# Kernel optimization log

Hardware: AMD Instinct MI355X
Metric: run time of the kernel (lower is better)

The kernel has to match this reference:

```python
import jax, jax.numpy as jnp
import numpy as np

D, H, L, FF, IN, OUT, S, B = 512, 8, 6, 2048, 32, 3, 512, 32


def setup_inputs() -> dict:
    key = jax.random.key(0)
    ks = iter(jax.random.split(key, 32))
    w = lambda shape: jax.random.normal(next(ks), shape, jnp.float32) * 0.02
    z = lambda shape: jnp.zeros(shape, jnp.float32)
    o = lambda shape: jnp.ones(shape, jnp.float32)
    return {
        'x': jax.random.normal(next(ks), (B, S, IN), jnp.float32),
        'w_in': w((IN, D)), 'b_in': z((D,)), 'g_in': o((D,)), 'be_in': z((D,)),
        'w_qkv': w((L, D, 3 * D)), 'b_qkv': z((L, 3 * D)),
        'w_out': w((L, D, D)), 'b_out': z((L, D)),
        'g1': o((L, D)), 'be1': z((L, D)),
        'w_ff1': w((L, D, FF)), 'b_ff1': z((L, FF)),
        'w_ff2': w((L, FF, D)), 'b_ff2': z((L, D)),
        'g2': o((L, D)), 'be2': z((L, D)),
        'w_h1': w((D, D // 2)), 'b_h1': z((D // 2,)),
        'w_h2': w((D // 2, OUT)), 'b_h2': z((OUT,)),
    }


def _layer_norm(x, g, b, eps=1e-5):
    mu = jnp.mean(x, axis=-1, keepdims=True)
    var = jnp.mean(jnp.square(x - mu), axis=-1, keepdims=True)
    return (x - mu) / jnp.sqrt(var + eps) * g + b


def _gelu(x):
    return jax.nn.gelu(x, approximate=False)  # torch nn.GELU default (erf)


def _pos_encoding(seq_len, d_model):
    pos = jnp.arange(seq_len, dtype=jnp.float32)[:, None]
    div = jnp.exp(jnp.arange(0, d_model, 2, dtype=jnp.float32) * (-np.log(10000.0) / d_model))
    pe = jnp.zeros((seq_len, d_model), jnp.float32)
    pe = pe.at[:, 0::2].set(jnp.sin(pos * div))
    pe = pe.at[:, 1::2].set(jnp.cos(pos * div))
    return pe


def reference(x, w_in, b_in, g_in, be_in, w_qkv, b_qkv, w_out, b_out,
              g1, be1, w_ff1, b_ff1, w_ff2, b_ff2, g2, be2,
              w_h1, b_h1, w_h2, b_h2):
    b, s, _ = x.shape
    d = w_in.shape[1]
    hd = d // H
    scale = hd ** -0.5

    # input projection: Linear -> LayerNorm -> GELU (dropout = identity at eval)
    h = _gelu(_layer_norm(x @ w_in + b_in, g_in, be_in))
    h = h + _pos_encoding(s, d)

    causal_mask = jnp.triu(jnp.ones((s, s), bool), 1)  # True above diagonal = future

    for l in range(w_qkv.shape[0]):
        qkv = (h @ w_qkv[l] + b_qkv[l]).reshape(b, s, 3, H, hd)
        q, k, v = qkv[:, :, 0], qkv[:, :, 1], qkv[:, :, 2]  # [b, s, H, hd]
        scores = jnp.einsum('bihd,bjhd->bhij', q, k) * scale
        scores = jnp.where(causal_mask, -jnp.inf, scores)
        attn = jax.nn.softmax(scores, axis=-1)
        o = jnp.einsum('bhij,bjhd->bihd', attn, v).reshape(b, s, d)
        o = o @ w_out[l] + b_out[l]
        h = _layer_norm(h + o, g1[l], be1[l])
        f = _gelu(h @ w_ff1[l] + b_ff1[l]) @ w_ff2[l] + b_ff2[l]
        h = _layer_norm(h + f, g2[l], be2[l])

    logits = _gelu(h @ w_h1 + b_h1) @ w_h2 + b_h2  # [b, s, OUT]
    return logits[:, -1, :]  # last position only
```

## Files before the change

### kernel.cpp

```cpp
#include <hip/hip_runtime.h>
#include <hip/hip_bf16.h>
#include <math.h>

#define D_   512
#define H_   8
#define HD_  64
#define L_   6
#define FF_  2048
#define IN_  32
#define OUT_ 3
#define S_   512
#define B_   32
#define M_   (B_ * S_)

typedef __attribute__((ext_vector_type(8))) short short8;
typedef __attribute__((ext_vector_type(4))) float floatx4;

__device__ __forceinline__ float gelu_f(float x) {
    const float ax = fabsf(x) * 0.70710678118654752f;
    const float t = __builtin_amdgcn_rcpf(fmaf(0.3275911f, ax, 1.0f));
    float p = fmaf(1.061405429f, t, -1.453152027f);
    p = fmaf(p, t, 1.421413741f);
    p = fmaf(p, t, -0.284496736f);
    p = fmaf(p, t, 0.254829592f);
    p = p * t;
    const float e = __expf(-ax * ax);
    const float er = copysignf(fmaf(-p, e, 1.0f), x);
    return 0.5f * x * (1.0f + er);
}
__device__ __forceinline__ float bf2f(unsigned short u) {
    union { unsigned int i; float f; } c; c.i = ((unsigned)u) << 16; return c.f;
}
__device__ __forceinline__ unsigned short f2bf(float v) {
    __hip_bfloat16 t = __float2bfloat16(v);
    return *(unsigned short*)&t;
}
__device__ __forceinline__ void async16(const void* g, void* l) {
    __builtin_amdgcn_global_load_lds(
        (const __attribute__((address_space(1))) unsigned int*)g,
        (__attribute__((address_space(3))) unsigned int*)l, 16, 0, 0);
}
__device__ __forceinline__ void stage2(const short* g, char* d, long rs, int off2) {
    async16(g, d);
    async16(g + rs, d + off2);
}


#define MFMA_ROW(ai, accr)                                                    \
    accr[0] = __builtin_amdgcn_mfma_f32_16x16x32_bf16(ai, b[0], accr[0], 0, 0, 0); \
    accr[1] = __builtin_amdgcn_mfma_f32_16x16x32_bf16(ai, b[1], accr[1], 0, 0, 0); \
    accr[2] = __builtin_amdgcn_mfma_f32_16x16x32_bf16(ai, b[2], accr[2], 0, 0, 0); \
    accr[3] = __builtin_amdgcn_mfma_f32_16x16x32_bf16(ai, b[3], accr[3], 0, 0, 0);

#define MFMA_PHASE(B0)                                                        \
    __builtin_amdgcn_s_barrier();                                             \
    asm volatile("s_waitcnt lgkmcnt(0)" ::: "memory");                        \
    __builtin_amdgcn_sched_barrier(0);                                        \
    __builtin_amdgcn_s_setprio(1);                                            \
    MFMA_ROW(a[0], acc[B0 + 0])                                               \
    MFMA_ROW(a[1], acc[B0 + 1])                                               \
    MFMA_ROW(a[2], acc[B0 + 2])                                               \
    MFMA_ROW(a[3], acc[B0 + 3])                                               \
    __builtin_amdgcn_s_setprio(0);

template<int DO_GELU, int OUT_BF16, int ADD_RES>
__global__ __launch_bounds__(512, 2)
void gemm_mfma256_k(const __hip_bfloat16* __restrict__ A,
                    const __hip_bfloat16* __restrict__ WT,
                    const float* __restrict__ bias,
                    const float* __restrict__ R,
                    void* __restrict__ C,
                    int N, int K) {
    __shared__ __align__(16) char smem[131072];

    const int tid  = threadIdx.x;
    const int lane = tid & 63;
    const int wave = tid >> 6;

    const int Lid = blockIdx.y * gridDim.x + blockIdx.x;
    const int xcd = Lid & 7;
    const int idx = Lid >> 3;
    const int gx  = gridDim.x, gy8 = gridDim.y >> 3;
    const int m0 = (xcd * gy8 + idx / gx) * 256;
    const int n0 = (idx % gx) * 256;

    const int wm = (wave >> 2) * 128;
    const int wn = (wave & 3) * 64;
    const int r = lane & 15, q = lane >> 4;
    const int qa = (q ^ ((r >> 1) & 3)) * 8;

    const int srow = tid >> 2;
    const int sc = ((tid & 3) ^ ((tid >> 3) & 3)) * 8;
    const short* Ag = (const short*)A + (long)(m0 + srow) * K + sc;
    const short* Bg = (const short*)WT + (long)(n0 + srow) * K + sc;
    const long rs = (long)128 * K;

    floatx4 acc[8][4];
    #pragma unroll
    for (int i = 0; i < 8; i++)
        #pragma unroll
        for (int j = 0; j < 4; j++) acc[i][j] = (floatx4)0.f;

    const int NT = K >> 6;

    stage2(Ag,      smem         + tid * 16, rs, 8192);
    stage2(Bg,      smem + 32768 + tid * 16, rs, 8192);
    stage2(Ag + 32, smem + 16384 + tid * 16, rs, 8192);
    stage2(Bg + 32, smem + 49152 + tid * 16, rs, 8192);
    asm volatile("s_waitcnt vmcnt(4)" ::: "memory");
    __builtin_amdgcn_s_barrier();

    short8 a[4], b[4];
    for (int t = 0; t < NT; ++t) {
        const int cur = t & 1, nxt = cur ^ 1;
        const bool hn = (t + 1 < NT);
        const short* As = (const short*)(smem + cur * 65536);
        const short* Bs = (const short*)(smem + cur * 65536 + 32768);
        const short* Agt = Ag + (t + 1) * 64;
        const short* Bgt = Bg + (t + 1) * 64;
        char* Ad = smem + nxt * 65536;
        char* Bd = smem + nxt * 65536 + 32768;

        #pragma unroll
        for (int i = 0; i < 4; i++)
            a[i] = *(const short8*)&As[(wm + i * 16 + r) * 32 + qa];
        #pragma unroll
        for (int j = 0; j < 4; j++)
            b[j] = *(const short8*)&Bs[(wn + j * 16 + r) * 32 + qa];
        if (hn) stage2(Agt, Ad + tid * 16, rs, 8192);
        MFMA_PHASE(0)
        __builtin_amdgcn_s_barrier();

        #pragma unroll
        for (int i = 0; i < 4; i++)
            a[i] = *(const short8*)&As[(wm + 64 + i * 16 + r) * 32 + qa];
        if (hn) stage2(Bgt, Bd + tid * 16, rs, 8192);
        MFMA_PHASE(4)
        if (hn) asm volatile("s_waitcnt vmcnt(4)" ::: "memory");
        else    asm volatile("s_waitcnt vmcnt(0)" ::: "memory");
        __builtin_amdgcn_s_barrier();

        #pragma unroll
        for (int i = 0; i < 4; i++)
            a[i] = *(const short8*)&As[8192 + (wm + i * 16 + r) * 32 + qa];
        #pragma unroll
        for (int j = 0; j < 4; j++)
            b[j] = *(const short8*)&Bs[8192 + (wn + j * 16 + r) * 32 + qa];
        if (hn) stage2(Agt + 32, Ad + 16384 + tid * 16, rs, 8192);
        MFMA_PHASE(0)
        __builtin_amdgcn_s_barrier();

        #pragma unroll
        for (int i = 0; i < 4; i++)
            a[i] = *(const short8*)&As[8192 + (wm + 64 + i * 16 + r) * 32 + qa];
        if (hn) stage2(Bgt + 32, Bd + 16384 + tid * 16, rs, 8192);
        MFMA_PHASE(4)
        if (hn) asm volatile("s_waitcnt vmcnt(4)" ::: "memory");
        __builtin_amdgcn_s_barrier();
    }

    float* Ef = (float*)smem;
    const int erow = tid >> 3;
    const int ej = tid & 7;
    #pragma unroll
    for (int ch = 0; ch < 4; ch++) {
        __builtin_amdgcn_s_barrier();
        if ((wave >> 2) == (ch >> 1)) {
            #pragma unroll
            for (int mf2 = 0; mf2 < 4; mf2++) {
                const int mf = (ch & 1) * 4 + mf2;
                #pragma unroll
                for (int nf = 0; nf < 4; nf++)
                    #pragma unroll
                    for (int rg = 0; rg < 4; rg++)
                        Ef[(mf2 * 16 + q * 4 + rg) * 260 + wn + nf * 16 + r] =
                            acc[mf][nf][rg];
            }
        }
        __builtin_amdgcn_s_barrier();
        #pragma unroll
        for (int e = 0; e < 8; e++) {
            const int c4 = ej + e * 8;
            const long grow = (long)(m0 + ch * 64 + erow) * N + n0 + c4 * 4;
            const float4 v = *(const float4*)&Ef[erow * 260 + c4 * 4];
            const float4 bv = *(const float4*)&bias[n0 + c4 * 4];
            float o0 = v.x + bv.x, o1 = v.y + bv.y;
            float o2 = v.z + bv.z, o3 = v.w + bv.w;
            if (DO_GELU) {
                o0 = gelu_f(o0); o1 = gelu_f(o1);
                o2 = gelu_f(o2); o3 = gelu_f(o3);
            }
            if (ADD_RES) {
                const float4 rv = *(const float4*)&R[grow];
                o0 += rv.x; o1 += rv.y; o2 += rv.z; o3 += rv.w;
            }
            if (OUT_BF16) {
                ushort4 pk;
                pk.x = f2bf(o0); pk.y = f2bf(o1);
                pk.z = f2bf(o2); pk.w = f2bf(o3);
                *(ushort4*)((unsigned short*)C + grow) = pk;
            } else {
                *(float4*)((float*)C + grow) = make_float4(o0, o1, o2, o3);
            }
        }
    }
}

template<int DO_GELU, int OUT_BF16, int ADD_RES>
__global__ __launch_bounds__(256, 2)
void gemm_mfma_k(const __hip_bfloat16* __restrict__ A,
                 const __hip_bfloat16* __restrict__ WT,
                 const float* __restrict__ bias,
                 const float* __restrict__ R,
                 void* __restrict__ C,
                 int N, int K) {
    __shared__ __align__(16) char smem[65536];
    float* Ep = (float*)smem;

    const int tid  = threadIdx.x;
    const int lane = tid & 63;
    const int wave = tid >> 6;

    const int Lid = blockIdx.y * gridDim.x + blockIdx.x;
    const int xcd = Lid & 7;
    const int idx = Lid >> 3;
    const int gx  = gridDim.x, gy8 = gridDim.y >> 3;
    const int m0 = (xcd * gy8 + idx / gx) * 128;
    const int n0 = (idx % gx) * 128;

    const int wm = (wave >> 1) * 64, wn = (wave & 1) * 64;
    const int r = lane & 15, q = lane >> 4;
    const int qa = (q ^ ((r >> 1) & 3)) * 8;

    const int srow = tid >> 2;
    const int sc = ((tid & 3) ^ ((tid >> 3) & 3)) * 8;
    const short* Ag = (const short*)A + (long)(m0 + srow) * K + sc;
    const short* Bg = (const short*)WT + (long)(n0 + srow) * K + sc;
    const long rs = (long)64 * K;

    floatx4 acc[4][4];
    #pragma unroll
    for (int i = 0; i < 4; i++)
        #pragma unroll
        for (int j = 0; j < 4; j++) acc[i][j] = (floatx4)0.f;

    const int NT = K >> 6;

    stage2(Ag,      smem + 0     + tid * 16, rs, 4096);
    stage2(Bg,      smem + 16384 + tid * 16, rs, 4096);
    stage2(Ag + 32, smem + 8192  + tid * 16, rs, 4096);
    stage2(Bg + 32, smem + 24576 + tid * 16, rs, 4096);
    asm volatile("s_waitcnt vmcnt(4)" ::: "memory");
    __builtin_amdgcn_s_barrier();
    __builtin_amdgcn_sched_barrier(0);

    short8 a[4], b[4];
    for (int t = 0; t < NT; ++t) {
        const int cur = t & 1, nxt = cur ^ 1;
        const bool hn = (t + 1 < NT);
        const short* As = (const short*)(smem + cur * 32768);
        const short* Bs = (const short*)(smem + cur * 32768 + 16384);
        const short* Agt = Ag + (t + 1) * 64;
        const short* Bgt = Bg + (t + 1) * 64;
        char* Ad = smem + nxt * 32768;
        char* Bd = smem + nxt * 32768 + 16384;

        if (hn) {
            stage2(Agt, Ad + tid * 16, rs, 4096);
            stage2(Bgt, Bd + tid * 16, rs, 4096);
        }
        #pragma unroll
        for (int i = 0; i < 4; i++)
            a[i] = *(const short8*)&As[(wm + i * 16 + r) * 32 + qa];
        #pragma unroll
        for (int j = 0; j < 4; j++)
            b[j] = *(const short8*)&Bs[(wn + j * 16 + r) * 32 + qa];
        #pragma unroll
        for (int i = 0; i < 4; i++)
            #pragma unroll
            for (int j = 0; j < 4; j++)
                acc[i][j] = __builtin_amdgcn_mfma_f32_16x16x32_bf16(
                    a[i], b[j], acc[i][j], 0, 0, 0);
        __builtin_amdgcn_sched_barrier(0);
        if (hn) asm volatile("s_waitcnt vmcnt(4)" ::: "memory");
        else    asm volatile("s_waitcnt vmcnt(0)" ::: "memory");
        __builtin_amdgcn_s_barrier();
        __builtin_amdgcn_sched_barrier(0);

        if (hn) {
            stage2(Agt + 32, Ad + 8192 + tid * 16, rs, 4096);
            stage2(Bgt + 32, Bd + 8192 + tid * 16, rs, 4096);
        }
        #pragma unroll
        for (int i = 0; i < 4; i++)
            a[i] = *(const short8*)&As[4096 + (wm + i * 16 + r) * 32 + qa];
        #pragma unroll
        for (int j = 0; j < 4; j++)
            b[j] = *(const short8*)&Bs[4096 + (wn + j * 16 + r) * 32 + qa];
        #pragma unroll
        for (int i = 0; i < 4; i++)
            #pragma unroll
            for (int j = 0; j < 4; j++)
                acc[i][j] = __builtin_amdgcn_mfma_f32_16x16x32_bf16(
                    a[i], b[j], acc[i][j], 0, 0, 0);
        __builtin_amdgcn_sched_barrier(0);
        if (hn) asm volatile("s_waitcnt vmcnt(4)" ::: "memory");
        __builtin_amdgcn_s_barrier();
        __builtin_amdgcn_sched_barrier(0);
    }

    const int erow = tid >> 5;
    const int ecol = (tid & 31) * 4;
    const float4 bvec = *(const float4*)&bias[n0 + ecol];

    #pragma unroll
    for (int pass = 0; pass < 2; pass++) {
        if (pass) __syncthreads();
        if ((wave >> 1) == pass) {
            #pragma unroll
            for (int i = 0; i < 4; i++)
                #pragma unroll
                for (int j = 0; j < 4; j++)
                    #pragma unroll
                    for (int rg = 0; rg < 4; rg++)
                        Ep[(i * 16 + q * 4 + rg) * 132 + wn + j * 16 + r] =
                            acc[i][j][rg];
        }
        __syncthreads();
        #pragma unroll
        for (int it = 0; it < 8; it++) {
            const int row = it * 8 + erow;
            const long grow = (long)(m0 + pass * 64 + row) * N + n0 + ecol;
            const float4 v = *(const float4*)&Ep[row * 132 + ecol];
            float o0 = v.x + bvec.x, o1 = v.y + bvec.y;
            float o2 = v.z + bvec.z, o3 = v.w + bvec.w;
            if (DO_GELU) {
                o0 = gelu_f(o0); o1 = gelu_f(o1);
                o2 = gelu_f(o2); o3 = gelu_f(o3);
            }
            if (ADD_RES) {
                const float4 rv = *(const float4*)&R[grow];
                o0 += rv.x; o1 += rv.y; o2 += rv.z; o3 += rv.w;
            }
            if (OUT_BF16) {
                ushort4 pk;
                pk.x = f2bf(o0); pk.y = f2bf(o1);
                pk.z = f2bf(o2); pk.w = f2bf(o3);
                *(ushort4*)((unsigned short*)C + grow) = pk;
            } else {
                *(float4*)((float*)C + grow) = make_float4(o0, o1, o2, o3);
            }
        }
    }
}

__global__ __launch_bounds__(256)
void transpose_cast_k(const float* __restrict__ W, __hip_bfloat16* __restrict__ WT,
                      int K, int N) {
    __shared__ float tile[32][33];
    const float* Wl = W + (long)blockIdx.z * K * N;
    __hip_bfloat16* WTl = WT + (long)blockIdx.z * K * N;
    const int n0 = blockIdx.x * 32, k0 = blockIdx.y * 32;
    const int tx = threadIdx.x & 31, ty = threadIdx.x >> 5;
    for (int rr = ty; rr < 32; rr += 8)
        tile[rr][tx] = Wl[(long)(k0 + rr) * N + n0 + tx];
    __syncthreads();
    for (int rr = ty; rr < 32; rr += 8)
        WTl[(long)(n0 + rr) * K + k0 + tx] = __float2bfloat16(tile[tx][rr]);
}

template<int DO_GELU>
__global__ __launch_bounds__(256)
void gemm_bias_k(const float* __restrict__ A, long lda,
                 const float* __restrict__ W,
                 const float* __restrict__ bias,
                 float* __restrict__ C,
                 int M, int N, int K) {
    __shared__ float As[16][64];
    __shared__ float Ws[16][64];
    const int tx = threadIdx.x;
    const int ty = threadIdx.y;
    const int tid = ty * 16 + tx;
    const int m0 = blockIdx.y * 64;
    const int n0 = blockIdx.x * 64;
    float acc[4][4] = {};
    for (int k0 = 0; k0 < K; k0 += 16) {
        #pragma unroll
        for (int e = tid; e < 64 * 16; e += 256) {
            int m = e >> 4, k = e & 15;
            float v = 0.f;
            if (m0 + m < M) v = A[(long)(m0 + m) * lda + k0 + k];
            As[k][m] = v;
        }
        #pragma unroll
        for (int e = tid; e < 16 * 64; e += 256) {
            int k = e >> 6, n = e & 63;
            float v = 0.f;
            if (n0 + n < N) v = W[(long)(k0 + k) * N + n0 + n];
            Ws[k][n] = v;
        }
        __syncthreads();
        #pragma unroll
        for (int kk = 0; kk < 16; kk++) {
            float a[4], w[4];
            #pragma unroll
            for (int i = 0; i < 4; i++) a[i] = As[kk][ty * 4 + i];
            #pragma unroll
            for (int j = 0; j < 4; j++) w[j] = Ws[kk][tx * 4 + j];
            #pragma unroll
            for (int i = 0; i < 4; i++)
                #pragma unroll
                for (int j = 0; j < 4; j++)
                    acc[i][j] += a[i] * w[j];
        }
        __syncthreads();
    }
    #pragma unroll
    for (int i = 0; i < 4; i++) {
        int m = m0 + ty * 4 + i;
        if (m >= M) continue;
        #pragma unroll
        for (int j = 0; j < 4; j++) {
            int n = n0 + tx * 4 + j;
            if (n >= N) continue;
            float v = acc[i][j] + bias[n];
            if (DO_GELU) v = gelu_f(v);
            C[(long)m * N + n] = v;
        }
    }
}

__global__ __launch_bounds__(256)
void ln_k(const float* __restrict__ X,
          const float* __restrict__ g,
          const float* __restrict__ be,
          float* __restrict__ H,
          __hip_bfloat16* __restrict__ Hb) {
    const int row = blockIdx.x * 4 + (threadIdx.x >> 6);
    const int lane = threadIdx.x & 63;
    const float* xp = X + (long)row * D_ + lane * 8;
    const float4 a = *(const float4*)xp;
    const float4 c = *(const float4*)(xp + 4);
    float s = a.x + a.y + a.z + a.w + c.x + c.y + c.z + c.w;
    #pragma unroll
    for (int off = 1; off < 64; off <<= 1) s += __shfl_xor(s, off);
    const float mu = s * (1.0f / D_);
    float d[8] = { a.x - mu, a.y - mu, a.z - mu, a.w - mu,
                   c.x - mu, c.y - mu, c.z - mu, c.w - mu };
    float ss = 0.f;
    #pragma unroll
    for (int e = 0; e < 8; e++) ss += d[e] * d[e];
    #pragma unroll
    for (int off = 1; off < 64; off <<= 1) ss += __shfl_xor(ss, off);
    const float inv = 1.0f / sqrtf(ss * (1.0f / D_) + 1e-5f);
    const float4 g0 = *(const float4*)(g + lane * 8);
    const float4 g1 = *(const float4*)(g + lane * 8 + 4);
    const float4 e0 = *(const float4*)(be + lane * 8);
    const float4 e1 = *(const float4*)(be + lane * 8 + 4);
    const float gv[8] = { g0.x, g0.y, g0.z, g0.w, g1.x, g1.y, g1.z, g1.w };
    const float ev[8] = { e0.x, e0.y, e0.z, e0.w, e1.x, e1.y, e1.z, e1.w };
    float o[8];
    short8 pk;
    #pragma unroll
    for (int e = 0; e < 8; e++) {
        o[e] = d[e] * inv * gv[e] + ev[e];
        pk[e] = (short)f2bf(o[e]);
    }
    float* hp = H + (long)row * D_ + lane * 8;
    *(float4*)hp = make_float4(o[0], o[1], o[2], o[3]);
    *(float4*)(hp + 4) = make_float4(o[4], o[5], o[6], o[7]);
    *(short8*)((unsigned short*)Hb + (long)row * D_ + lane * 8) = pk;
}

__global__ __launch_bounds__(256)
void ln_gelu_pos_k(const float* __restrict__ X,
                   const float* __restrict__ g,
                   const float* __restrict__ be,
                   float* __restrict__ Hout,
                   __hip_bfloat16* __restrict__ Hb) {
    const int row = blockIdx.x;
    const int s = row & (S_ - 1);
    const int t = threadIdx.x;
    const float* x = X + (long)row * D_;
    float v0 = x[t], v1 = x[t + 256];
    __shared__ float red[256];
    red[t] = v0 + v1;
    __syncthreads();
    for (int off = 128; off; off >>= 1) {
        if (t < off) red[t] += red[t + off];
        __syncthreads();
    }
    float mu = red[0] * (1.0f / D_);
    __syncthreads();
    float d0 = v0 - mu, d1 = v1 - mu;
    red[t] = d0 * d0 + d1 * d1;
    __syncthreads();
    for (int off = 128; off; off >>= 1) {
        if (t < off) red[t] += red[t + off];
        __syncthreads();
    }
    float var = red[0] * (1.0f / D_);
    float inv = 1.0f / sqrtf(var + 1e-5f);
    float o0 = gelu_f(d0 * inv * g[t] + be[t]);
    float o1 = gelu_f(d1 * inv * g[t + 256] + be[t + 256]);
    {
        int d = t, i = d >> 1;
        float dv = expf((float)(2 * i) * (-9.210340371976184f / 512.0f));
        float ang = (float)s * dv;
        o0 += (d & 1) ? cosf(ang) : sinf(ang);
    }
    {
        int d = t + 256, i = d >> 1;
        float dv = expf((float)(2 * i) * (-9.210340371976184f / 512.0f));
        float ang = (float)s * dv;
        o1 += (d & 1) ? cosf(ang) : sinf(ang);
    }
    Hout[(long)row * D_ + t] = o0;
    Hout[(long)row * D_ + t + 256] = o1;
    Hb[(long)row * D_ + t] = __float2bfloat16(o0);
    Hb[(long)row * D_ + t + 256] = __float2bfloat16(o1);
}

#define LDT 72
__global__ __launch_bounds__(256)
void attn_mfma_k(const __hip_bfloat16* __restrict__ qkv,
                 __hip_bfloat16* __restrict__ O) {
    const int qt = blockIdx.x;
    const int bh = blockIdx.y;
    const int b = bh >> 3, h = bh & (H_ - 1);
    const int tid = threadIdx.x;
    const int wave = tid >> 6, lane = tid & 63;
    const int ln = lane & 15, quad = lane >> 4;
    const int wm = wave * 32;
    const int i0 = qt * 128;

    __shared__ unsigned short Qs[128 * LDT];
    __shared__ unsigned short Ks[64 * LDT];
    __shared__ unsigned short Vt[64 * LDT];
    __shared__ unsigned short Ps[128 * LDT];
    __shared__ float stat[128];

    const unsigned short* base = (const unsigned short*)qkv + (long)b * S_ * (3 * D_);

    {
        const int r0 = tid >> 3, c0 = (tid & 7) * 8;
        #pragma unroll
        for (int i = 0; i < 4; i++) {
            const int rw = i * 32 + r0;
            *(short8*)&Qs[rw * LDT + c0] =
                *(const short8*)(base + (long)(i0 + rw) * (3 * D_) + h * HD_ + c0);
        }
    }

    float m_i[2] = { -INFINITY, -INFINITY };
    float l_i[2] = { 0.f, 0.f };
    floatx4 o_acc[2][4];
    #pragma unroll
    for (int i = 0; i < 2; i++)
        #pragma unroll
        for (int j = 0; j < 4; j++) o_acc[i][j] = (floatx4)0.f;

    const int kr = tid >> 2, kc = (tid & 3) * 16;
    const int vj = tid & 63, vc = (tid >> 6) * 16;

    const int ktmax = 2 * qt + 1;
    for (int kt = 0; kt <= ktmax; kt++) {
        const int j0 = kt * 64;
        {
            const unsigned short* kp = base + (long)(j0 + kr) * (3 * D_) + D_ + h * HD_ + kc;
            *(short8*)&Ks[kr * LDT + kc]     = *(const short8*)(kp);
            *(short8*)&Ks[kr * LDT + kc + 8] = *(const short8*)(kp + 8);
            const unsigned short* vp = base + (long)(j0 + vj) * (3 * D_) + 2 * D_ + h * HD_ + vc;
            short8 v0 = *(const short8*)(vp);
            short8 v1 = *(const short8*)(vp + 8);
            #pragma unroll
            for (int e = 0; e < 8; e++) {
                Vt[(vc + e) * LDT + vj]     = (unsigned short)v0[e];
                Vt[(vc + 8 + e) * LDT + vj] = (unsigned short)v1[e];
            }
        }
        __syncthreads();

        floatx4 sa[4][2];
        #pragma unroll
        for (int mt = 0; mt < 4; mt++)
            #pragma unroll
            for (int nt = 0; nt < 2; nt++) sa[mt][nt] = (floatx4)0.f;
        #pragma unroll
        for (int c = 0; c < 2; c++) {
            short8 kf[4], qf[2];
            #pragma unroll
            for (int mt = 0; mt < 4; mt++)
                kf[mt] = *(const short8*)&Ks[(mt * 16 + ln) * LDT + c * 32 + quad * 8];
            #pragma unroll
            for (int nt = 0; nt < 2; nt++)
                qf[nt] = *(const short8*)&Qs[(wm + nt * 16 + ln) * LDT + c * 32 + quad * 8];
            #pragma unroll
            for (int mt = 0; mt < 4; mt++)
                #pragma unroll
                for (int nt = 0; nt < 2; nt++)
                    sa[mt][nt] = __builtin_amdgcn_mfma_f32_16x16x32_bf16(
                        kf[mt], qf[nt], sa[mt][nt], 0, 0, 0);
        }

        const bool domask = (kt >= 2 * qt);
        #pragma unroll
        for (int nt = 0; nt < 2; nt++) {
            const int qg = i0 + wm + nt * 16 + ln;
            float mx = -INFINITY;
            #pragma unroll
            for (int mt = 0; mt < 4; mt++)
                #pragma unroll
                for (int rg = 0; rg < 4; rg++) {
                    float v = sa[mt][nt][rg] * 0.125f;
                    if (domask && (j0 + mt * 16 + quad * 4 + rg > qg)) v = -INFINITY;
                    sa[mt][nt][rg] = v;
                    mx = fmaxf(mx, v);
                }
            mx = fmaxf(mx, __shfl_xor(mx, 16));
            mx = fmaxf(mx, __shfl_xor(mx, 32));
            const float mn = fmaxf(m_i[nt], mx);
            const float alpha = __expf(m_i[nt] - mn);
            m_i[nt] = mn;
            float ls = 0.f;
            #pragma unroll
            for (int mt = 0; mt < 4; mt++) {
                ushort4 pk;
                float p0 = __expf(sa[mt][nt][0] - mn);
                float p1 = __expf(sa[mt][nt][1] - mn);
                float p2 = __expf(sa[mt][nt][2] - mn);
                float p3 = __expf(sa[mt][nt][3] - mn);
                ls += p0 + p1 + p2 + p3;
                pk.x = f2bf(p0); pk.y = f2bf(p1); pk.z = f2bf(p2); pk.w = f2bf(p3);
                *(ushort4*)&Ps[(wm + nt * 16 + ln) * LDT + mt * 16 + quad * 4] = pk;
            }
            ls += __shfl_xor(ls, 16);
            ls += __shfl_xor(ls, 32);
            l_i[nt] = l_i[nt] * alpha + ls;
            if (quad == 0) stat[wm + nt * 16 + ln] = alpha;
        }

        #pragma unroll
        for (int mt2 = 0; mt2 < 2; mt2++) {
            #pragma unroll
            for (int rg = 0; rg < 4; rg++) {
                const float a = stat[wm + mt2 * 16 + quad * 4 + rg];
                #pragma unroll
                for (int nt = 0; nt < 4; nt++) o_acc[mt2][nt][rg] *= a;
            }
        }

        #pragma unroll
        for (int c = 0; c < 2; c++) {
            short8 pf[2], vf[4];
            #pragma unroll
            for (int mt2 = 0; mt2 < 2; mt2++)
                pf[mt2] = *(const short8*)&Ps[(wm + mt2 * 16 + ln) * LDT + c * 32 + quad * 8];
            #pragma unroll
            for (int nt = 0; nt < 4; nt++)
                vf[nt] = *(const short8*)&Vt[(nt * 16 + ln) * LDT + c * 32 + quad * 8];
            #pragma unroll
            for (int mt2 = 0; mt2 < 2; mt2++)
                #pragma unroll
                for (int nt = 0; nt < 4; nt++)
                    o_acc[mt2][nt] = __builtin_amdgcn_mfma_f32_16x16x32_bf16(
                        pf[mt2], vf[nt], o_acc[mt2][nt], 0, 0, 0);
        }
        __syncthreads();
    }

    if (quad == 0) {
        stat[wm + ln]      = l_i[0];
        stat[wm + 16 + ln] = l_i[1];
    }
    unsigned short* Og = (unsigned short*)O;
    #pragma unroll
    for (int mt2 = 0; mt2 < 2; mt2++) {
        #pragma unroll
        for (int rg = 0; rg < 4; rg++) {
            const float linv = 1.0f / stat[wm + mt2 * 16 + quad * 4 + rg];
            const long row = (long)(b * S_ + i0 + wm + mt2 * 16 + quad * 4 + rg);
            #pragma unroll
            for (int nt = 0; nt < 4; nt++)
                Og[row * D_ + h * HD_ + nt * 16 + ln] =
                    f2bf(o_acc[mt2][nt][rg] * linv);
        }
    }
}

__global__ __launch_bounds__(256)
void head1_k(const float* __restrict__ h, const float* __restrict__ w1,
             const float* __restrict__ b1, float* __restrict__ th) {
    __shared__ float hs[D_];
    const int b = blockIdx.x, n = threadIdx.x;
    const float* hr = h + (long)(b * S_ + S_ - 1) * D_;
    hs[n] = hr[n];
    hs[n + 256] = hr[n + 256];
    __syncthreads();
    float s = 0.f;
    #pragma unroll 8
    for (int k = 0; k < D_; k++) s += hs[k] * w1[(long)k * 256 + n];
    th[b * 256 + n] = gelu_f(s + b1[n]);
}

__global__ __launch_bounds__(64)
void head2_k(const float* __restrict__ th, const float* __restrict__ w2,
             const float* __restrict__ b2, float* __restrict__ out) {
    const int b = blockIdx.x, lane = threadIdx.x;
    const float* t = th + b * 256;
    float s0 = 0.f, s1 = 0.f, s2 = 0.f;
    #pragma unroll
    for (int e = 0; e < 4; e++) {
        const int k = lane * 4 + e;
        const float tv = t[k];
        s0 += tv * w2[k * 3 + 0];
        s1 += tv * w2[k * 3 + 1];
        s2 += tv * w2[k * 3 + 2];
    }
    #pragma unroll
    for (int off = 1; off < 64; off <<= 1) {
        s0 += __shfl_xor(s0, off);
        s1 += __shfl_xor(s1, off);
        s2 += __shfl_xor(s2, off);
    }
    if (lane == 0) {
        out[b * 3 + 0] = s0 + b2[0];
        out[b * 3 + 1] = s1 + b2[1];
        out[b * 3 + 2] = s2 + b2[2];
    }
}

extern "C" void kernel_launch(void* const* d_in, const int* in_sizes, int n_in,
                              void* d_out, int out_size, void* d_ws, size_t ws_size,
                              hipStream_t stream) {
    const float* x     = (const float*)d_in[0];
    const float* w_in  = (const float*)d_in[1];
    const float* b_in  = (const float*)d_in[2];
    const float* g_in  = (const float*)d_in[3];
    const float* be_in = (const float*)d_in[4];
    const float* w_qkv = (const float*)d_in[5];
    const float* b_qkv = (const float*)d_in[6];
    const float* w_out = (const float*)d_in[7];
    const float* b_out = (const float*)d_in[8];
    const float* g1    = (const float*)d_in[9];
    const float* be1   = (const float*)d_in[10];
    const float* w_ff1 = (const float*)d_in[11];
    const float* b_ff1 = (const float*)d_in[12];
    const float* w_ff2 = (const float*)d_in[13];
    const float* b_ff2 = (const float*)d_in[14];
    const float* g2    = (const float*)d_in[15];
    const float* be2   = (const float*)d_in[16];
    const float* w_h1  = (const float*)d_in[17];
    const float* b_h1  = (const float*)d_in[18];
    const float* w_h2  = (const float*)d_in[19];
    const float* b_h2  = (const float*)d_in[20];
    float* out = (float*)d_out;

    float* h    = (float*)d_ws;
    float* bufB = h + (long)M_ * D_;
    float* th   = bufB + (long)M_ * D_;
    __hip_bfloat16* hb    = (__hip_bfloat16*)(th + 32 * 256);
    __hip_bfloat16* attb  = hb + (long)M_ * D_;
    __hip_bfloat16* bufAb = attb + (long)M_ * D_;
    __hip_bfloat16* qkvT  = bufAb + (long)M_ * FF_;
    __hip_bfloat16* outT  = qkvT + (long)L_ * (3 * D_) * D_;
    __hip_bfloat16* ff1T  = outT + (long)L_ * D_ * D_;
    __hip_bfloat16* ff2T  = ff1T + (long)L_ * FF_ * D_;

    dim3 blk(16, 16);

    transpose_cast_k<<<dim3((3 * D_) / 32, D_ / 32, L_), 256, 0, stream>>>(w_qkv, qkvT, D_, 3 * D_);
    transpose_cast_k<<<dim3(D_ / 32, D_ / 32, L_), 256, 0, stream>>>(w_out, outT, D_, D_);
    transpose_cast_k<<<dim3(FF_ / 32, D_ / 32, L_), 256, 0, stream>>>(w_ff1, ff1T, D_, FF_);
    transpose_cast_k<<<dim3(D_ / 32, FF_ / 32, L_), 256, 0, stream>>>(w_ff2, ff2T, FF_, D_);

    gemm_bias_k<0><<<dim3(D_ / 64, M_ / 64), blk, 0, stream>>>(
        x, IN_, w_in, b_in, bufB, M_, D_, IN_);
    ln_gelu_pos_k<<<M_, 256, 0, stream>>>(bufB, g_in, be_in, h, hb);

    for (int l = 0; l < L_; l++) {
        gemm_mfma_k<0, 1, 0><<<dim3((3 * D_) / 128, M_ / 128), 256, 0, stream>>>(
            hb, qkvT + (long)l * (3 * D_) * D_, b_qkv + l * 3 * D_, nullptr,
            bufAb, 3 * D_, D_);
        attn_mfma_k<<<dim3(S_ / 128, B_ * H_), 256, 0, stream>>>(bufAb, attb);
        gemm_mfma_k<0, 0, 1><<<dim3(D_ / 128, M_ / 128), 256, 0, stream>>>(
            attb, outT + (long)l * D_ * D_, b_out + l * D_, h,
            bufB, D_, D_);
        ln_k<<<M_ / 4, 256, 0, stream>>>(bufB, g1 + l * D_, be1 + l * D_, h, hb);
        gemm_mfma256_k<1, 1, 0><<<dim3(FF_ / 256, M_ / 256), 512, 0, stream>>>(
            hb, ff1T + (long)l * FF_ * D_, b_ff1 + l * FF_, nullptr,
            bufAb, FF_, D_);
        gemm_mfma_k<0, 0, 1><<<dim3(D_ / 128, M_ / 128), 256, 0, stream>>>(
            bufAb, ff2T + (long)l * D_ * FF_, b_ff2 + l * D_, h,
            bufB, D_, FF_);
        ln_k<<<M_ / 4, 256, 0, stream>>>(bufB, g2 + l * D_, be2 + l * D_, h, hb);
    }

    head1_k<<<B_, 256, 0, stream>>>(h, w_h1, b_h1, th);
    head2_k<<<B_, 64, 0, stream>>>(th, w_h2, b_h2, out);
}
```

Measured before the change: 1.688 ms.

## Fuse output/FF2 projection GEMMs with residual add and LayerNorm

Adds a GEMM kernel that computes full 64x512 output rows per block, so bias, residual add and LayerNorm run in the epilogue and write both fp32 and bf16 hidden states. It replaces the separate GEMM plus ln_k launches after attention and after FF2, removing the fp32 intermediate round trip and two launches per layer. In exchange it uses 256 blocks with about 144KB of LDS and one block per CU, so occupancy drops, and the layout is hardcoded to D=512. The residual R and the output Hout alias the same buffer h; this is safe only because each block reads its own rows before writing them.

```diff
diff --git a/kernel.cpp b/kernel.cpp
--- a/kernel.cpp
+++ b/kernel.cpp
@@ -350,6 +350,176 @@
             } else {
                 *(float4*)((float*)C + grow) = make_float4(o0, o1, o2, o3);
             }
+        }
+    }
+}
+
+__global__ __launch_bounds__(512, 1)
+void gemm_ln_k(const __hip_bfloat16* __restrict__ A,
+               const __hip_bfloat16* __restrict__ WT,
+               const float* __restrict__ bias,
+               const float* R,
+               const float* __restrict__ g,
+               const float* __restrict__ be,
+               float* Hout,
+               __hip_bfloat16* __restrict__ Hb,
+               int K) {
+    __shared__ __align__(16) char smem[147456];
+    const int tid  = threadIdx.x;
+    const int lane = tid & 63;
+    const int wave = tid >> 6;
+
+    const int Lid = blockIdx.x;
+    const int m0 = ((Lid & 7) * 32 + (Lid >> 3)) * 64;
+
+    const int wm2 = wave >> 2;
+    const int wn4 = wave & 3;
+    const int r = lane & 15, q = lane >> 4;
+    const int qaB  = (q ^ ((r >> 1) & 3)) * 8;
+    const int qaA0 = ((q)     ^ (r & 7)) * 8;
+    const int qaA1 = ((4 + q) ^ (r & 7)) * 8;
+
+    const int arow = tid >> 3;
+    const int asb  = ((tid & 7) ^ ((tid >> 3) & 7)) * 8;
+    const short* Ag = (const short*)A + (long)(m0 + arow) * K + asb;
+    const int brow = tid >> 2;
+    const int bsb  = ((tid & 3) ^ ((tid >> 3) & 3)) * 8;
+    const short* Bg = (const short*)WT + (long)brow * K + bsb;
+    const long brs = (long)128 * K;
+
+    floatx4 acc[2][8];
+    #pragma unroll
+    for (int i = 0; i < 2; i++)
+        #pragma unroll
+        for (int j = 0; j < 8; j++) acc[i][j] = (floatx4)0.f;
+
+    const int NTT = K >> 6;
+
+    {
+        char* base = smem;
+        async16(Ag, base + tid * 16);
+        const short* p0 = Bg;
+        char* d0 = base + 8192 + tid * 16;
+        async16(p0, d0); async16(p0 + brs, d0 + 8192);
+        async16(p0 + 2 * brs, d0 + 16384); async16(p0 + 3 * brs, d0 + 24576);
+        const short* p1 = Bg + 32;
+        char* d1 = base + 40960 + tid * 16;
+        async16(p1, d1); async16(p1 + brs, d1 + 8192);
+        async16(p1 + 2 * brs, d1 + 16384); async16(p1 + 3 * brs, d1 + 24576);
+    }
+    asm volatile("s_waitcnt vmcnt(4)" ::: "memory");
+    __builtin_amdgcn_s_barrier();
+    __builtin_amdgcn_sched_barrier(0);
+
+    for (int t = 0; t < NTT; ++t) {
+        const int cur = t & 1, nxt = cur ^ 1;
+        const bool hn = (t + 1 < NTT);
+        const short* As  = (const short*)(smem + cur * 73728);
+        const short* B0s = (const short*)(smem + cur * 73728 + 8192);
+        const short* B1s = (const short*)(smem + cur * 73728 + 40960);
+        char* nb = smem + nxt * 73728;
+        const long k1 = (long)(t + 1) * 64;
+
+        if (hn) {
+            async16(Ag + k1, nb + tid * 16);
+            const short* p0 = Bg + k1;
+            char* d0 = nb + 8192 + tid * 16;
+            async16(p0, d0); async16(p0 + brs, d0 + 8192);
+            async16(p0 + 2 * brs, d0 + 16384); async16(p0 + 3 * brs, d0 + 24576);
+        }
+        {
+            short8 a0 = *(const short8*)&As[(wm2 * 32 +      r) * 64 + qaA0];
+            short8 a1 = *(const short8*)&As[(wm2 * 32 + 16 + r) * 64 + qaA0];
+            short8 b[8];
+            #pragma unroll
+            for (int nf = 0; nf < 8; nf++)
+                b[nf] = *(const short8*)&B0s[(wn4 * 128 + nf * 16 + r) * 32 + qaB];
+            #pragma unroll
+            for (int nf = 0; nf < 8; nf++) {
+                acc[0][nf] = __builtin_amdgcn_mfma_f32_16x16x32_bf16(a0, b[nf], acc[0][nf], 0, 0, 0);
+                acc[1][nf] = __builtin_amdgcn_mfma_f32_16x16x32_bf16(a1, b[nf], acc[1][nf], 0, 0, 0);
+            }
+        }
+        __builtin_amdgcn_sched_barrier(0);
+        if (hn) asm volatile("s_waitcnt vmcnt(4)" ::: "memory");
+        else    asm volatile("s_waitcnt vmcnt(0)" ::: "memory");
+        __builtin_amdgcn_s_barrier();
+        __builtin_amdgcn_sched_barrier(0);
+
+        if (hn) {
+            const short* p1 = Bg + k1 + 32;
+            char* d1 = nb + 40960 + tid * 16;
+            async16(p1, d1); async16(p1 + brs, d1 + 8192);
+            async16(p1 + 2 * brs, d1 + 16384); async16(p1 + 3 * brs, d1 + 24576);
+        }
+        {
+            short8 a0 = *(const short8*)&As[(wm2 * 32 +      r) * 64 + qaA1];
+            short8 a1 = *(const short8*)&As[(wm2 * 32 + 16 + r) * 64 + qaA1];
+            short8 b[8];
+            #pragma unroll
+            for (int nf = 0; nf < 8; nf++)
+                b[nf] = *(const short8*)&B1s[(wn4 * 128 + nf * 16 + r) * 32 + qaB];
+            #pragma unroll
+            for (int nf = 0; nf < 8; nf++) {
+                acc[0][nf] = __builtin_amdgcn_mfma_f32_16x16x32_bf16(a0, b[nf], acc[0][nf], 0, 0, 0);
+                acc[1][nf] = __builtin_amdgcn_mfma_f32_16x16x32_bf16(a1, b[nf], acc[1][nf], 0, 0, 0);
+            }
+        }
+        __builtin_amdgcn_sched_barrier(0);
+        if (hn) asm volatile("s_waitcnt vmcnt(4)" ::: "memory");
+        __builtin_amdgcn_s_barrier();
+        __builtin_amdgcn_sched_barrier(0);
+    }
+
+    float* Ef = (float*)smem;
+    float* stat = (float*)(smem + 66816);
+    const float gl = g[tid], bl = be[tid], bv = bias[tid];
+
+    #pragma unroll
+    for (int ch = 0; ch < 2; ch++) {
+        if (ch) __syncthreads();
+        if (wm2 == ch) {
+            #pragma unroll
+            for (int mf = 0; mf < 2; mf++)
+                #pragma unroll
+                for (int nf = 0; nf < 8; nf++)
+                    #pragma unroll
+                    for (int rg = 0; rg < 4; rg++)
+                        Ef[(mf * 16 + q * 4 + rg) * 522 + wn4 * 128 + nf * 16 + r] =
+                            acc[mf][nf][rg];
+        }
+        __syncthreads();
+        const int gm = m0 + ch * 32;
+        #pragma unroll 8
+        for (int k = 0; k < 32; k++)
+            Ef[k * 522 + tid] += bv + R[(long)(gm + k) * 512 + tid];
+        __syncthreads();
+        {
+            const int row = tid >> 4, cc = tid & 15;
+            float s = 0.f, ss = 0.f;
+            #pragma unroll 8
+            for (int j = 0; j < 32; j++) {
+                const float v = Ef[row * 522 + cc + 16 * j];
+                s += v; ss += v * v;
+            }
+            #pragma unroll
+            for (int off = 1; off < 16; off <<= 1) {
+                s  += __shfl_xor(s, off);
+                ss += __shfl_xor(ss, off);
+            }
+            const float mu  = s * (1.0f / 512.0f);
+            const float var = fmaxf(ss * (1.0f / 512.0f) - mu * mu, 0.f);
+            const float inv = 1.0f / sqrtf(var + 1e-5f);
+            if (cc == 0) { stat[row * 2] = mu; stat[row * 2 + 1] = inv; }
+        }
+        __syncthreads();
+        #pragma unroll 8
+        for (int k = 0; k < 32; k++) {
+            const float v  = Ef[k * 522 + tid];
+            const float o  = (v - stat[k * 2]) * stat[k * 2 + 1] * gl + bl;
+            const long idx = (long)(gm + k) * 512 + tid;
+            Hout[idx] = o;
+            ((unsigned short*)Hb)[idx] = f2bf(o);
         }
     }
 }
@@ -783,17 +953,15 @@
             hb, qkvT + (long)l * (3 * D_) * D_, b_qkv + l * 3 * D_, nullptr,
             bufAb, 3 * D_, D_);
         attn_mfma_k<<<dim3(S_ / 128, B_ * H_), 256, 0, stream>>>(bufAb, attb);
-        gemm_mfma_k<0, 0, 1><<<dim3(D_ / 128, M_ / 128), 256, 0, stream>>>(
+        gemm_ln_k<<<256, 512, 0, stream>>>(
             attb, outT + (long)l * D_ * D_, b_out + l * D_, h,
-            bufB, D_, D_);
-        ln_k<<<M_ / 4, 256, 0, stream>>>(bufB, g1 + l * D_, be1 + l * D_, h, hb);
+            g1 + l * D_, be1 + l * D_, h, hb, D_);
         gemm_mfma256_k<1, 1, 0><<<dim3(FF_ / 256, M_ / 256), 512, 0, stream>>>(
             hb, ff1T + (long)l * FF_ * D_, b_ff1 + l * FF_, nullptr,
             bufAb, FF_, D_);
-        gemm_mfma_k<0, 0, 1><<<dim3(D_ / 128, M_ / 128), 256, 0, stream>>>(
+        gemm_ln_k<<<256, 512, 0, stream>>>(
             bufAb, ff2T + (long)l * D_ * FF_, b_ff2 + l * D_, h,
-            bufB, D_, FF_);
-        ln_k<<<M_ / 4, 256, 0, stream>>>(bufB, g2 + l * D_, be2 + l * D_, h, hb);
+            g2 + l * D_, be2 + l * D_, h, hb, FF_);
     }
 
     head1_k<<<B_, 256, 0, stream>>>(h, w_h1, b_h1, th);
```

Result: faster. 1.638 ms (-2.9%).
